# Kernel tuning notes

Measured on AMD Instinct MI355X. Metric: run time of the kernel, lower is better.

Reference implementation:

```python
import jax, jax.numpy as jnp
import numpy as np

N, E, B = 100000, 400000, 4096      # nodes, directed edges, graphs
P, d = 4, 49                        # phm_dim, per-component dim; D = P*d = 196
L = 3                               # message-passing layers
D1, D2 = 64, 32                     # downstream per-component dims (256/4, 128/4)


def setup_inputs():
    key = jax.random.key(0)
    ks = jax.random.split(key, 20)
    def nrm(k, shape, s=0.1):
        return jax.random.normal(k, shape, dtype=jnp.float32) * s
    return {
        "x": jax.random.randint(ks[0], (N, 9), 0, 119),
        "edge_index": jax.random.randint(ks[1], (2, E), 0, N),
        "edge_attr": jax.random.randint(ks[2], (E, 3), 0, 8),
        "batch": jnp.sort(jax.random.randint(ks[3], (N,), 0, B)),
        # encoders: summed categorical embeddings in hypercomplex form [*, P, d]
        "atom_emb": nrm(ks[4], (9, 119, P, d)),
        "bond_emb": nrm(ks[5], (L, 3, 8, P, d)),
        # per-layer PHM conv: contribution matrices A (phm rule) + component weights W
        "conv_A": nrm(ks[6], (L, P, P, P), 0.5),
        "conv_W": nrm(ks[7], (L, P, d, d)),
        "conv_b": jnp.zeros((L, P, d), jnp.float32),
        "mp_gamma": jnp.ones((L, P * d), jnp.float32),
        "mp_beta": jnp.zeros((L, P * d), jnp.float32),
        # soft-attention pooling: PHM linear + real transformer gate
        "pool_A": nrm(ks[8], (P, P, P), 0.5),
        "pool_W": nrm(ks[9], (P, d, d)),
        "pool_b": jnp.zeros((P, d), jnp.float32),
        "pool_rt_w": nrm(ks[10], (P,), 0.5),
        "pool_rt_b": jnp.zeros((d,), jnp.float32),
        # downstream PHM MLP 196 -> 256 -> 128 -> 4*1, then real trafo -> 1
        "dn_A": nrm(ks[11], (3, P, P, P), 0.5),
        "dn1_W": nrm(ks[12], (P, d, D1)),
        "dn1_b": jnp.zeros((P, D1), jnp.float32),
        "dn1_gamma": jnp.ones((P * D1,), jnp.float32),
        "dn1_beta": jnp.zeros((P * D1,), jnp.float32),
        "dn2_W": nrm(ks[13], (P, D1, D2)),
        "dn2_b": jnp.zeros((P, D2), jnp.float32),
        "dn2_gamma": jnp.ones((P * D2,), jnp.float32),
        "dn2_beta": jnp.zeros((P * D2,), jnp.float32),
        "dn3_W": nrm(ks[14], (P, D2, 1)),
        "dn3_b": jnp.zeros((P, 1), jnp.float32),
        "rt_w": nrm(ks[15], (P,), 0.5),
        "rt_b": jnp.zeros((1,), jnp.float32),
    }


def phm_linear(x, A, W, b):
    # PHM linear: y = x @ (sum_i kron(A_i, W_i)) + b, on [n, P, din] -> [n, P, dout]
    return jnp.einsum('nkp,ikj,ipq->njq', x, A, W) + b


def naive_bn(x, gamma, beta, eps=1e-5):
    # naive batch norm over the batch axis, per flattened hypercomplex feature
    n, p, dd = x.shape
    x2 = x.reshape(n, p * dd)
    mu = x2.mean(axis=0)
    var = x2.var(axis=0)
    x2 = (x2 - mu) * jax.lax.rsqrt(var + eps) * gamma + beta
    return x2.reshape(n, p, dd)


def reference(x, edge_index, edge_attr, batch, atom_emb, bond_emb,
              conv_A, conv_W, conv_b, mp_gamma, mp_beta,
              pool_A, pool_W, pool_b, pool_rt_w, pool_rt_b,
              dn_A, dn1_W, dn1_b, dn1_gamma, dn1_beta,
              dn2_W, dn2_b, dn2_gamma, dn2_beta, dn3_W, dn3_b, rt_w, rt_b):
    src, dst = edge_index[0], edge_index[1]
    # atom encoder: sum embeddings of 9 categorical features -> [N, P, d]
    h0 = atom_emb[jnp.arange(9), x].sum(axis=1)
    h = h0
    for l in range(L):  # small fixed layer count
        # bond encoder for this layer -> [E, P, d]
        e = bond_emb[l][jnp.arange(3), edge_attr].sum(axis=1)
        # message = x_j + e_ij (identity msg encoder); self-loop (zero edge feat) adds h
        m = h[src] + e
        agg = jax.ops.segment_sum(m, dst, num_segments=N) + h
        z = phm_linear(agg, conv_A[l], conv_W[l], conv_b[l])
        z = jax.nn.relu(naive_bn(z, mp_gamma[l], mp_beta[l]))
        h = z + h0  # skip-connect to first embedding (sc_type='first')
    # soft-attention pooling: real-valued sigmoid gate per node feature
    g = jax.nn.sigmoid(
        jnp.einsum('npk,p->nk', phm_linear(h, pool_A, pool_W, pool_b), pool_rt_w)
        + pool_rt_b)
    pooled = jax.ops.segment_sum(h * g[:, None, :], batch, num_segments=B)  # [B, P, d]
    # downstream PHM MLP with naive batch norm + relu
    z = jax.nn.relu(naive_bn(phm_linear(pooled, dn_A[0], dn1_W, dn1_b), dn1_gamma, dn1_beta))
    z = jax.nn.relu(naive_bn(phm_linear(z, dn_A[1], dn2_W, dn2_b), dn2_gamma, dn2_beta))
    o = phm_linear(z, dn_A[2], dn3_W, dn3_b)          # [B, P, 1]
    return jnp.einsum('npk,p->nk', o, rt_w) + rt_b    # [B, 1]
```

## Files before the change

### kernel.cpp

```cpp
#include <hip/hip_runtime.h>
#include <cstdint>
#include <cstddef>

#define N_NODES 100000
#define N_EDGES 400000
#define N_GRAPHS 4096
#define DF 196
#define DD 49
#define NPB 5
#define TST 200

typedef __bf16 bf16x8 __attribute__((ext_vector_type(8)));
typedef float f32x4 __attribute__((ext_vector_type(4)));

__device__ __forceinline__ unsigned short f2bf(float f) {
  unsigned int u = __float_as_uint(f);
  u = u + 0x7FFFu + ((u >> 16) & 1u);
  return (unsigned short)(u >> 16);
}
__device__ __forceinline__ float bf2f(unsigned short h) {
  return __uint_as_float(((unsigned int)h) << 16);
}

__global__ void convert_wfrag_kernel(const float* __restrict__ cA,
                                     const float* __restrict__ cW,
                                     unsigned short* __restrict__ wfrag) {
  int idx = blockIdx.x * blockDim.x + threadIdx.x;
  if (idx >= 3 * 100352) return;
  int l = idx / 100352;
  int r = idx - l * 100352;
  int ct = r / 7168; int r1 = r - ct * 7168;
  int ks = r1 / 1024; int r2 = r1 - ks * 1024;
  int h = r2 / 512;  int r3 = r2 - h * 512;
  int ln = r3 / 8;   int j = r3 - ln * 8;
  int col = ct * 16 + (ln & 15);
  int k = ks * 32 + (ln >> 4) * 8 + j;
  float v = 0.f;
  if (col < DF && k < DF) {
    int k4 = k / DD, p = k - (k / DD) * DD;
    int j4 = col / DD, q = col - (col / DD) * DD;
#pragma unroll
    for (int i = 0; i < 4; i++)
      v += cA[((l * 4 + i) * 4 + k4) * 4 + j4] * cW[((l * 4 + i) * DD + p) * DD + q];
  }
  unsigned short hi = f2bf(v);
  wfrag[idx] = (h == 0) ? hi : f2bf(v - bf2f(hi));
}

__global__ void build_gate_kernel(const float* __restrict__ pA, const float* __restrict__ pW,
                                  const float* __restrict__ pb, const float* __restrict__ rtw,
                                  const float* __restrict__ rtb,
                                  float* __restrict__ gateW, float* __restrict__ gbias) {
  int idx = blockIdx.x * blockDim.x + threadIdx.x;
  if (idx < DF * DD) {
    int r = idx / DD, q = idx - (idx / DD) * DD;
    int k = r / DD, p = r - (r / DD) * DD;
    float s = 0.f;
#pragma unroll
    for (int i = 0; i < 4; i++) {
      float aw = 0.f;
#pragma unroll
      for (int j = 0; j < 4; j++) aw += pA[(i * 4 + k) * 4 + j] * rtw[j];
      s += aw * pW[(i * DD + p) * DD + q];
    }
    gateW[idx] = s;
  } else if (idx < DF * DD + DD) {
    int q = idx - DF * DD;
    float s = rtb[q];
#pragma unroll
    for (int j = 0; j < 4; j++) s += rtw[j] * pb[j * DD + q];
    gbias[q] = s;
  }
}

__global__ void build_dn_kernel(const float* __restrict__ dnA,
                                const float* __restrict__ W1, const float* __restrict__ W2,
                                const float* __restrict__ W3,
                                float* __restrict__ M1, float* __restrict__ M2,
                                float* __restrict__ M3) {
  int idx = blockIdx.x * blockDim.x + threadIdx.x;
  const int n1 = DF * 256, n2 = 256 * 128, n3 = 128 * 4;
  if (idx < n1) {
    int r = idx >> 8, c = idx & 255;
    int k = r / DD, p = r - (r / DD) * DD;
    int j = c >> 6, Q = c & 63;
    float s = 0.f;
#pragma unroll
    for (int i = 0; i < 4; i++) s += dnA[i * 16 + k * 4 + j] * W1[(i * DD + p) * 64 + Q];
    M1[idx] = s;
  } else if (idx < n1 + n2) {
    int m = idx - n1;
    int r = m >> 7, c = m & 127;
    int k = r >> 6, p = r & 63, j = c >> 5, q = c & 31;
    float s = 0.f;
#pragma unroll
    for (int i = 0; i < 4; i++) s += dnA[64 + i * 16 + k * 4 + j] * W2[(i * 64 + p) * 32 + q];
    M2[m] = s;
  } else if (idx < n1 + n2 + n3) {
    int m = idx - n1 - n2;
    int r = m >> 2, j = m & 3;
    int k = r >> 5, p = r & 31;
    float s = 0.f;
#pragma unroll
    for (int i = 0; i < 4; i++) s += dnA[128 + i * 16 + k * 4 + j] * W3[i * 32 + p];
    M3[m] = s;
  }
}

__global__ void lut_kernel(const float* __restrict__ bond, float* __restrict__ lut) {
  int idx = blockIdx.x * blockDim.x + threadIdx.x;
  if (idx >= 3 * 512 * DF) return;
  int l = idx / (512 * DF);
  int r = idx - l * (512 * DF);
  int code = r / DF, c = r - (r / DF) * DF;
  int a0 = code & 7, a1 = (code >> 3) & 7, a2 = (code >> 6) & 7;
  lut[idx] = bond[((l * 3 + 0) * 8 + a0) * DF + c]
           + bond[((l * 3 + 1) * 8 + a1) * DF + c]
           + bond[((l * 3 + 2) * 8 + a2) * DF + c];
}

__global__ void hist_kernel(const int* __restrict__ dst, int* __restrict__ counts) {
  int e = blockIdx.x * blockDim.x + threadIdx.x;
  if (e < N_EDGES) atomicAdd(&counts[dst[e]], 1);
}

__global__ void scan_local_kernel(const int* __restrict__ counts, int* __restrict__ offs,
                                  int* __restrict__ bsum) {
  __shared__ int sm[256];
  int tid = threadIdx.x;
  int gid = blockIdx.x * 256 + tid;
  int v = (gid < N_NODES) ? counts[gid] : 0;
  sm[tid] = v;
  __syncthreads();
  for (int d = 1; d < 256; d <<= 1) {
    int add = (tid >= d) ? sm[tid - d] : 0;
    __syncthreads();
    sm[tid] += add;
    __syncthreads();
  }
  if (gid < N_NODES) offs[gid] = sm[tid] - v;
  if (tid == 255) bsum[blockIdx.x] = sm[255];
}

__global__ void scan_bsum_kernel(int* __restrict__ bsum, int* __restrict__ bpre, int nb) {
  __shared__ int sm[512];
  int tid = threadIdx.x;
  int v = (tid < nb) ? bsum[tid] : 0;
  sm[tid] = v;
  __syncthreads();
  for (int d = 1; d < 512; d <<= 1) {
    int add = (tid >= d) ? sm[tid - d] : 0;
    __syncthreads();
    sm[tid] += add;
    __syncthreads();
  }
  if (tid < nb) bpre[tid] = sm[tid] - v;
}

__global__ void add_off_kernel(int* __restrict__ offs, const int* __restrict__ bpre) {
  int gid = blockIdx.x * blockDim.x + threadIdx.x;
  if (gid < N_NODES) offs[gid] += bpre[gid >> 8];
  if (gid == 0) offs[N_NODES] = N_EDGES;
}

__global__ void scatter_kernel(const int* __restrict__ src, const int* __restrict__ dst,
                               const int* __restrict__ ea, int* __restrict__ counts,
                               const int* __restrict__ offs,
                               unsigned int* __restrict__ sorted) {
  int e = blockIdx.x * blockDim.x + threadIdx.x;
  if (e >= N_EDGES) return;
  int d = dst[e];
  int code = ea[e * 3 + 0] | (ea[e * 3 + 1] << 3) | (ea[e * 3 + 2] << 6);
  int pos = offs[d] + atomicSub(&counts[d], 1) - 1;
  sorted[pos] = (unsigned int)src[e] | ((unsigned int)code << 17);
}

__global__ void sortseg_kernel(const int* __restrict__ offs,
                               unsigned int* __restrict__ sorted) {
  int n = blockIdx.x * blockDim.x + threadIdx.x;
  if (n >= N_NODES) return;
  int s = offs[n], e = offs[n + 1];
  for (int i = s + 1; i < e; i++) {
    unsigned int v = sorted[i];
    int j = i - 1;
    while (j >= s && sorted[j] > v) { sorted[j + 1] = sorted[j]; j--; }
    sorted[j + 1] = v;
  }
}

__global__ void atom_enc_kernel(const int* __restrict__ x, const float* __restrict__ emb,
                                float* __restrict__ h0) {
  int idx = blockIdx.x * blockDim.x + threadIdx.x;
  if (idx >= N_NODES * DF) return;
  int n = idx / DF;
  int c = idx - n * DF;
  float s = 0.f;
#pragma unroll
  for (int f = 0; f < 9; f++) {
    int xi = x[n * 9 + f];
    s += emb[(f * 119 + xi) * DF + c];
  }
  h0[idx] = s;
}

__global__ __launch_bounds__(256)
void agg_kernel(const float* __restrict__ h, const int* __restrict__ offs,
                const unsigned int* __restrict__ sorted, const float* __restrict__ lut,
                unsigned short* __restrict__ tH, unsigned short* __restrict__ tL) {
  int t = threadIdx.x;
  int i = t / 49, q = t - i * 49;
  if (i >= NPB) return;
  int node = blockIdx.x * NPB + i;
  if (node >= N_NODES) return;
  const float4* h4 = (const float4*)h;
  const float4* l4 = (const float4*)lut;
  float4 acc = h4[(size_t)node * 49 + q];
  int s = offs[node], e = offs[node + 1];
  for (int k = s; k < e; k++) {
    unsigned int se = sorted[k];
    int srcn = se & 0x1FFFF;
    int code = se >> 17;
    float4 hv = h4[(size_t)srcn * 49 + q];
    float4 lv = l4[(size_t)code * 49 + q];
    acc.x += hv.x + lv.x;
    acc.y += hv.y + lv.y;
    acc.z += hv.z + lv.z;
    acc.w += hv.w + lv.w;
  }
  ushort4 hh, ll;
  hh.x = f2bf(acc.x); ll.x = f2bf(acc.x - bf2f(hh.x));
  hh.y = f2bf(acc.y); ll.y = f2bf(acc.y - bf2f(hh.y));
  hh.z = f2bf(acc.z); ll.z = f2bf(acc.z - bf2f(hh.z));
  hh.w = f2bf(acc.w); ll.w = f2bf(acc.w - bf2f(hh.w));
  size_t ob = (size_t)node * TST + q * 4;
  *(ushort4*)(tH + ob) = hh;
  *(ushort4*)(tL + ob) = ll;
  if (q == 48) {
    ushort4 z = make_ushort4(0, 0, 0, 0);
    *(ushort4*)(tH + (size_t)node * TST + 196) = z;
    *(ushort4*)(tL + (size_t)node * TST + 196) = z;
  }
}

__global__ __launch_bounds__(256, 2)
void conv_mfma_kernel(unsigned short* __restrict__ tH,
                      unsigned short* __restrict__ tL,
                      const unsigned short* __restrict__ wfrag,
                      const float* __restrict__ bias,
                      float* __restrict__ stats) {
  __shared__ __align__(16) unsigned short smW[28672];
  const int t = threadIdx.x;
  const int lane = t & 63;
  const int w = t >> 6;
  const int li = lane & 15;
  const int rg = lane >> 4;
  const int rowbase = blockIdx.x * 128 + w * 32;

  f32x4 acc[2][14];
#pragma unroll
  for (int rt = 0; rt < 2; rt++)
#pragma unroll
    for (int ct = 0; ct < 14; ct++) acc[rt][ct] = (f32x4){0.f, 0.f, 0.f, 0.f};

  uint4 aH0[2], aL0[2], aH1[2], aL1[2];

#define LOADA(ks, aH, aL)                                                      \
  {                                                                            \
    _Pragma("unroll") for (int rt = 0; rt < 2; rt++) {                         \
      size_t o = (size_t)(rowbase + rt * 16 + li) * TST + (ks) * 32 + rg * 8;  \
      aH[rt] = *(const uint4*)(tH + o);                                        \
      aL[rt] = *(const uint4*)(tL + o);                                        \
    }                                                                          \
  }

#define COMPUTE(ksl, aH, aL)                                                   \
  {                                                                            \
    _Pragma("unroll") for (int ct = 0; ct < 14; ct++) {                        \
      bf16x8 bh = *(const bf16x8*)(smW + (((ct * 2 + (ksl)) * 2 + 0) * 512 + lane * 8)); \
      bf16x8 bl = *(const bf16x8*)(smW + (((ct * 2 + (ksl)) * 2 + 1) * 512 + lane * 8)); \
      _Pragma("unroll") for (int rt = 0; rt < 2; rt++) {                       \
        bf16x8 ah = *(const bf16x8*)&aH[rt];                                   \
        bf16x8 al = *(const bf16x8*)&aL[rt];                                   \
        acc[rt][ct] = __builtin_amdgcn_mfma_f32_16x16x32_bf16(ah, bh, acc[rt][ct], 0, 0, 0); \
        acc[rt][ct] = __builtin_amdgcn_mfma_f32_16x16x32_bf16(al, bh, acc[rt][ct], 0, 0, 0); \
        acc[rt][ct] = __builtin_amdgcn_mfma_f32_16x16x32_bf16(ah, bl, acc[rt][ct], 0, 0, 0); \
      }                                                                        \
    }                                                                          \
  }

#define STAGE_PAIR(p)                                                          \
  {                                                                            \
    _Pragma("unroll") for (int f0 = 0; f0 < 14; f0++) {                        \
      int f = f0 * 256 + t;                                                    \
      int ln = f & 63, g = f >> 6;                                             \
      int hh = g & 1, g2 = g >> 1;                                             \
      int ksl = g2 & 1, ct = g2 >> 1;                                          \
      *(uint4*)(smW + (((ct * 2 + ksl) * 2 + hh) * 512 + ln * 8)) =            \
          *(const uint4*)(wfrag + (((size_t)(ct * 7 + 2 * (p) + ksl) * 2 + hh) * 512 + ln * 8)); \
    }                                                                          \
  }

  LOADA(0, aH0, aL0);
  STAGE_PAIR(0);
  __syncthreads();
  LOADA(1, aH1, aL1);
  COMPUTE(0, aH0, aL0);
  LOADA(2, aH0, aL0);
  COMPUTE(1, aH1, aL1);
  __syncthreads();
  STAGE_PAIR(1);
  __syncthreads();
  LOADA(3, aH1, aL1);
  COMPUTE(0, aH0, aL0);
  LOADA(4, aH0, aL0);
  COMPUTE(1, aH1, aL1);
  __syncthreads();
  STAGE_PAIR(2);
  __syncthreads();
  LOADA(5, aH1, aL1);
  COMPUTE(0, aH0, aL0);
  LOADA(6, aH0, aL0);
  COMPUTE(1, aH1, aL1);
  __syncthreads();
  {
#pragma unroll
    for (int f0 = 0; f0 < 7; f0++) {
      int f = f0 * 256 + t;
      int ln = f & 63, g = f >> 6;
      int hh = g & 1, ct = g >> 1;
      *(uint4*)(smW + (((ct * 2) * 2 + hh) * 512 + ln * 8)) =
          *(const uint4*)(wfrag + (((size_t)(ct * 7 + 6) * 2 + hh) * 512 + ln * 8));
    }
  }
  __syncthreads();
  COMPUTE(0, aH0, aL0);
  __syncthreads();

  float* redS = (float*)smW;
  float* redQ = redS + 4 * 224;
#pragma unroll
  for (int ct = 0; ct < 14; ct++) {
    int c = ct * 16 + li;
    float bv = (c < DF) ? bias[c] : 0.f;
    float part = 0.f, psq = 0.f;
#pragma unroll
    for (int rt = 0; rt < 2; rt++) {
#pragma unroll
      for (int r = 0; r < 4; r++) {
        int gr = rowbase + rt * 16 + rg * 4 + r;
        float y = acc[rt][ct][r] + bv;
        if (gr < N_NODES && c < DF) {
          part += y; psq += y * y;
          unsigned short hi = f2bf(y);
          unsigned short lo = f2bf(y - bf2f(hi));
          size_t ob = (size_t)gr * TST + c;
          tH[ob] = hi;
          tL[ob] = lo;
        }
      }
    }
    part += __shfl_xor(part, 16, 64); part += __shfl_xor(part, 32, 64);
    psq  += __shfl_xor(psq , 16, 64); psq  += __shfl_xor(psq , 32, 64);
    if (rg == 0) { redS[w * 224 + c] = part; redQ[w * 224 + c] = psq; }
  }
  __syncthreads();
  if (t < DF) {
    float s1 = redS[t] + redS[224 + t] + redS[448 + t] + redS[672 + t];
    float s2 = redQ[t] + redQ[224 + t] + redQ[448 + t] + redQ[672 + t];
    atomicAdd(&stats[t], s1);
    atomicAdd(&stats[DF + t], s2);
  }
#undef LOADA
#undef COMPUTE
#undef STAGE_PAIR
}

__global__ void bn_relu_split_kernel(const unsigned short* __restrict__ tH,
                                     const unsigned short* __restrict__ tL,
                                     const float* __restrict__ stats,
                                     const float* __restrict__ gamma,
                                     const float* __restrict__ beta,
                                     const float* __restrict__ h0,
                                     float* __restrict__ h) {
  int idx = blockIdx.x * blockDim.x + threadIdx.x;
  if (idx >= N_NODES * DD) return;
  int n = idx / DD, q = idx - (idx / DD) * DD;
  size_t ib = (size_t)n * TST + q * 4;
  ushort4 hv = *(const ushort4*)(tH + ib);
  ushort4 lv = *(const ushort4*)(tL + ib);
  size_t fb = (size_t)n * DF + q * 4;
  float4 sk = *(const float4*)(h0 + fb);
  int c = q * 4;
  const float invN = 1.f / N_NODES;
  float4 o;
  {
    float z = bf2f(hv.x) + bf2f(lv.x);
    float mu = stats[c + 0] * invN;
    float var = stats[DF + c + 0] * invN - mu * mu;
    o.x = fmaxf((z - mu) * rsqrtf(var + 1e-5f) * gamma[c + 0] + beta[c + 0], 0.f) + sk.x;
  }
  {
    float z = bf2f(hv.y) + bf2f(lv.y);
    float mu = stats[c + 1] * invN;
    float var = stats[DF + c + 1] * invN - mu * mu;
    o.y = fmaxf((z - mu) * rsqrtf(var + 1e-5f) * gamma[c + 1] + beta[c + 1], 0.f) + sk.y;
  }
  {
    float z = bf2f(hv.z) + bf2f(lv.z);
    float mu = stats[c + 2] * invN;
    float var = stats[DF + c + 2] * invN - mu * mu;
    o.z = fmaxf((z - mu) * rsqrtf(var + 1e-5f) * gamma[c + 2] + beta[c + 2], 0.f) + sk.z;
  }
  {
    float z = bf2f(hv.w) + bf2f(lv.w);
    float mu = stats[c + 3] * invN;
    float var = stats[DF + c + 3] * invN - mu * mu;
    o.w = fmaxf((z - mu) * rsqrtf(var + 1e-5f) * gamma[c + 3] + beta[c + 3], 0.f) + sk.w;
  }
  *(float4*)(h + fb) = o;
}

template<int S, int MODE>
__launch_bounds__(256)
__global__ void gemm_kernel(const float* X, const float* __restrict__ W,
                            const float* __restrict__ bias, float* Y,
                            float* __restrict__ stats, int Nrows, int K, int NC) {
  constexpr int WN = S * 64;
  __shared__ __align__(16) float At[32][64];
  __shared__ __align__(16) float Wl[32][WN];
  const int t = threadIdx.x;
  const int tx = t & 15;
  const int ty = t >> 4;
  const int r0 = blockIdx.x * 64;

  float acc[S][4][4];
#pragma unroll
  for (int s = 0; s < S; s++)
#pragma unroll
    for (int i = 0; i < 4; i++)
#pragma unroll
      for (int j = 0; j < 4; j++) acc[s][i][j] = 0.f;

  const int lr = t >> 2;
  const int kb = (t & 3) * 8;
  constexpr int TPR = S * 16;
  const int cw = (t % TPR) * 4;
  const int kr = t / TPR;
  constexpr int RPP = 256 / TPR;
  constexpr int PASSES = 32 / RPP;

  for (int k0 = 0; k0 < K; k0 += 32) {
    {
      const int gr = r0 + lr;
      const float* xp = X + (size_t)gr * K + k0 + kb;
      if (gr < Nrows && (k0 + kb + 7) < K) {
        float4 v0 = *(const float4*)(xp);
        float4 v1 = *(const float4*)(xp + 4);
        At[kb + 0][lr] = v0.x; At[kb + 1][lr] = v0.y;
        At[kb + 2][lr] = v0.z; At[kb + 3][lr] = v0.w;
        At[kb + 4][lr] = v1.x; At[kb + 5][lr] = v1.y;
        At[kb + 6][lr] = v1.z; At[kb + 7][lr] = v1.w;
      } else {
#pragma unroll
        for (int i = 0; i < 8; i++) {
          int kk = kb + i;
          float v = 0.f;
          if (gr < Nrows && (k0 + kk) < K) v = xp[i];
          At[kk][lr] = v;
        }
      }
    }
#pragma unroll
    for (int ps = 0; ps < PASSES; ps++) {
      int kk = kr + ps * RPP;
      int gk = k0 + kk;
      if (gk < K && (cw + 3) < NC && ((NC & 3) == 0)) {
        float4 v = *(const float4*)(W + (size_t)gk * NC + cw);
        Wl[kk][cw + 0] = v.x; Wl[kk][cw + 1] = v.y;
        Wl[kk][cw + 2] = v.z; Wl[kk][cw + 3] = v.w;
      } else {
#pragma unroll
        for (int j = 0; j < 4; j++) {
          int c = cw + j;
          float v = 0.f;
          if (gk < K && c < NC) v = W[(size_t)gk * NC + c];
          Wl[kk][c] = v;
        }
      }
    }
    __syncthreads();
#pragma unroll 4
    for (int kk = 0; kk < 32; kk++) {
      float4 a = *(const float4*)&At[kk][ty * 4];
      float av[4] = {a.x, a.y, a.z, a.w};
#pragma unroll
      for (int s = 0; s < S; s++) {
        float4 w = *(const float4*)&Wl[kk][s * 64 + tx * 4];
        float wv[4] = {w.x, w.y, w.z, w.w};
#pragma unroll
        for (int i = 0; i < 4; i++)
#pragma unroll
          for (int j = 0; j < 4; j++)
            acc[s][i][j] = fmaf(av[i], wv[j], acc[s][i][j]);
      }
    }
    __syncthreads();
  }

#pragma unroll
  for (int s = 0; s < S; s++)
#pragma unroll
    for (int j = 0; j < 4; j++) {
      int c = s * 64 + tx * 4 + j;
      float bv = (c < NC) ? bias[c] : 0.f;
#pragma unroll
      for (int i = 0; i < 4; i++) {
        float y = acc[s][i][j] + bv;
        if (MODE == 1) y = 1.f / (1.f + __expf(-y));
        acc[s][i][j] = y;
      }
    }
#pragma unroll
  for (int i = 0; i < 4; i++) {
    int gr = r0 + ty * 4 + i;
    if (gr < Nrows) {
#pragma unroll
      for (int s = 0; s < S; s++)
#pragma unroll
        for (int j = 0; j < 4; j++) {
          int c = s * 64 + tx * 4 + j;
          if (c < NC) Y[(size_t)gr * NC + c] = acc[s][i][j];
        }
    }
  }
  if (MODE == 0) {
    float* red = &Wl[0][0];
    __syncthreads();
#pragma unroll
    for (int s = 0; s < S; s++)
#pragma unroll
      for (int j = 0; j < 4; j++) {
        float p = 0.f;
#pragma unroll
        for (int i = 0; i < 4; i++)
          if ((r0 + ty * 4 + i) < Nrows) p += acc[s][i][j];
        red[ty * WN + s * 64 + tx * 4 + j] = p;
      }
    __syncthreads();
    if (t < WN) {
      float tot = 0.f;
#pragma unroll
      for (int yy = 0; yy < 16; yy++) tot += red[yy * WN + t];
      if (t < NC) atomicAdd(&stats[t], tot);
    }
    __syncthreads();
#pragma unroll
    for (int s = 0; s < S; s++)
#pragma unroll
      for (int j = 0; j < 4; j++) {
        float p = 0.f;
#pragma unroll
        for (int i = 0; i < 4; i++)
          if ((r0 + ty * 4 + i) < Nrows) p += acc[s][i][j] * acc[s][i][j];
        red[ty * WN + s * 64 + tx * 4 + j] = p;
      }
    __syncthreads();
    if (t < WN) {
      float tot = 0.f;
#pragma unroll
      for (int yy = 0; yy < 16; yy++) tot += red[yy * WN + t];
      if (t < NC) atomicAdd(&stats[NC + t], tot);
    }
  }
}

__global__ void bn_relu_kernel(const float* __restrict__ z, const float* __restrict__ stats,
                               const float* __restrict__ gamma, const float* __restrict__ beta,
                               float* __restrict__ out,
                               int total, int NC, float invN) {
  int idx = blockIdx.x * blockDim.x + threadIdx.x;
  if (idx >= total) return;
  int c = idx % NC;
  float mu = stats[c] * invN;
  float var = stats[NC + c] * invN - mu * mu;
  float v = (z[idx] - mu) * rsqrtf(var + 1e-5f) * gamma[c] + beta[c];
  out[idx] = fmaxf(v, 0.f);
}

__device__ __forceinline__ int lower_bound_dev(const int* a, int n, int v) {
  int lo = 0, hi = n;
  while (lo < hi) { int mid = (lo + hi) >> 1; if (a[mid] < v) lo = mid + 1; else hi = mid; }
  return lo;
}

__global__ void pool_kernel(const float* __restrict__ h, const float* __restrict__ g,
                            const int* __restrict__ batch, float* __restrict__ pooled) {
  int b = blockIdx.x;
  __shared__ int bounds[2];
  if (threadIdx.x == 0) {
    bounds[0] = lower_bound_dev(batch, N_NODES, b);
    bounds[1] = lower_bound_dev(batch, N_NODES, b + 1);
  }
  __syncthreads();
  int c = threadIdx.x;
  if (c >= DF) return;
  int s = bounds[0], e = bounds[1];
  int q = c % DD;
  float acc = 0.f;
  for (int n = s; n < e; n++)
    acc = fmaf(h[(size_t)n * DF + c], g[(size_t)n * DD + q], acc);
  pooled[(size_t)b * DF + c] = acc;
}

__global__ void final_kernel(const float* __restrict__ z2, const float* __restrict__ M3,
                             const float* __restrict__ b3, const float* __restrict__ rtw,
                             const float* __restrict__ rtb, float* __restrict__ out) {
  __shared__ float sM[128 * 4];
  __shared__ float srw[4];
  __shared__ float srb;
  int t = threadIdx.x;
  for (int i = t; i < 512; i += 256) sM[i] = M3[i];
  if (t < 4) srw[t] = rtw[t];
  if (t == 4) srb = rtb[0];
  __syncthreads();
  int b = blockIdx.x * blockDim.x + t;
  if (b >= N_GRAPHS) return;
  float o0 = b3[0], o1 = b3[1], o2 = b3[2], o3 = b3[3];
  const float* zp = z2 + (size_t)b * 128;
  for (int p = 0; p < 128; p++) {
    float v = zp[p];
    o0 = fmaf(v, sM[p * 4 + 0], o0);
    o1 = fmaf(v, sM[p * 4 + 1], o1);
    o2 = fmaf(v, sM[p * 4 + 2], o2);
    o3 = fmaf(v, sM[p * 4 + 3], o3);
  }
  out[b] = srb + o0 * srw[0] + o1 * srw[1] + o2 * srw[2] + o3 * srw[3];
}

extern "C" void kernel_launch(void* const* d_in, const int* in_sizes, int n_in,
                              void* d_out, int out_size, void* d_ws, size_t ws_size,
                              hipStream_t stream) {
  (void)in_sizes; (void)n_in; (void)out_size; (void)ws_size;
  const int* x          = (const int*)d_in[0];
  const int* edge_index = (const int*)d_in[1];
  const int* edge_attr  = (const int*)d_in[2];
  const int* batch      = (const int*)d_in[3];
  const float* atom_emb = (const float*)d_in[4];
  const float* bond_emb = (const float*)d_in[5];
  const float* conv_A   = (const float*)d_in[6];
  const float* conv_W   = (const float*)d_in[7];
  const float* conv_b   = (const float*)d_in[8];
  const float* mp_gamma = (const float*)d_in[9];
  const float* mp_beta  = (const float*)d_in[10];
  const float* pool_A   = (const float*)d_in[11];
  const float* pool_W   = (const float*)d_in[12];
  const float* pool_b   = (const float*)d_in[13];
  const float* pool_rt_w = (const float*)d_in[14];
  const float* pool_rt_b = (const float*)d_in[15];
  const float* dn_A     = (const float*)d_in[16];
  const float* dn1_W    = (const float*)d_in[17];
  const float* dn1_b    = (const float*)d_in[18];
  const float* dn1_gamma = (const float*)d_in[19];
  const float* dn1_beta = (const float*)d_in[20];
  const float* dn2_W    = (const float*)d_in[21];
  const float* dn2_b    = (const float*)d_in[22];
  const float* dn2_gamma = (const float*)d_in[23];
  const float* dn2_beta = (const float*)d_in[24];
  const float* dn3_W    = (const float*)d_in[25];
  const float* dn3_b    = (const float*)d_in[26];
  const float* rt_w     = (const float*)d_in[27];
  const float* rt_b     = (const float*)d_in[28];
  float* out = (float*)d_out;

  char* ws = (char*)d_ws;
  size_t off = 0;
  auto alloc = [&](size_t bytes) -> char* {
    char* p = ws + off;
    off = (off + bytes + 255) & ~(size_t)255;
    return p;
  };
  const size_t HBYTES = (size_t)N_NODES * DF * sizeof(float);
  float* h0 = (float*)alloc(HBYTES);
  float* h  = (float*)alloc(HBYTES);
  unsigned short* tH = (unsigned short*)alloc((size_t)N_NODES * TST * 2 + 4096);
  unsigned short* tL = (unsigned short*)alloc((size_t)N_NODES * TST * 2 + 4096);
  float* g      = (float*)tH;
  float* pooled = (float*)((char*)tH + (((size_t)N_NODES * DD * 4 + 255) & ~(size_t)255));
  float* z1     = (float*)((char*)pooled + (((size_t)N_GRAPHS * DF * 4 + 255) & ~(size_t)255));
  float* z2     = (float*)((char*)z1 + (((size_t)N_GRAPHS * 256 * 4 + 255) & ~(size_t)255));
  unsigned short* wfrag = (unsigned short*)alloc((size_t)3 * 100352 * 2);
  float* gateW  = (float*)alloc(DF * DD * 4);
  float* gbias  = (float*)alloc(64 * 4);
  float* M1     = (float*)alloc(DF * 256 * 4);
  float* M2     = (float*)alloc(256 * 128 * 4);
  float* M3     = (float*)alloc(128 * 4 * 4);
  float* stats  = (float*)alloc(2048 * 4);
  int*  counts  = (int*)alloc(N_NODES * 4);
  int*  offs    = (int*)alloc((N_NODES + 1) * 4);
  unsigned int* sorted = (unsigned int*)alloc((size_t)N_EDGES * 4);
  float* lut    = (float*)alloc((size_t)3 * 512 * DF * 4);
  int*  bsum    = (int*)alloc(512 * 4);
  int*  bpre    = (int*)alloc(512 * 4);

  const int* src = edge_index;
  const int* dst = edge_index + N_EDGES;
  const int NB = (N_NODES + 255) / 256;

  hipMemsetAsync(stats, 0, 2048 * 4, stream);
  hipMemsetAsync(counts, 0, N_NODES * 4, stream);

  convert_wfrag_kernel<<<(3 * 100352 + 255) / 256, 256, 0, stream>>>(conv_A, conv_W, wfrag);
  build_gate_kernel<<<(DF * DD + DD + 255) / 256, 256, 0, stream>>>(
      pool_A, pool_W, pool_b, pool_rt_w, pool_rt_b, gateW, gbias);
  build_dn_kernel<<<(DF * 256 + 256 * 128 + 128 * 4 + 255) / 256, 256, 0, stream>>>(
      dn_A, dn1_W, dn2_W, dn3_W, M1, M2, M3);
  lut_kernel<<<(3 * 512 * DF + 255) / 256, 256, 0, stream>>>(bond_emb, lut);

  hist_kernel<<<(N_EDGES + 255) / 256, 256, 0, stream>>>(dst, counts);
  scan_local_kernel<<<NB, 256, 0, stream>>>(counts, offs, bsum);
  scan_bsum_kernel<<<1, 512, 0, stream>>>(bsum, bpre, NB);
  add_off_kernel<<<NB, 256, 0, stream>>>(offs, bpre);
  scatter_kernel<<<(N_EDGES + 255) / 256, 256, 0, stream>>>(
      src, dst, edge_attr, counts, offs, sorted);
  sortseg_kernel<<<NB, 256, 0, stream>>>(offs, sorted);

  atom_enc_kernel<<<(N_NODES * DF + 255) / 256, 256, 0, stream>>>(x, atom_emb, h0);

  const int NCONV = (N_NODES + 127) / 128;
  for (int l = 0; l < 3; l++) {
    const float* hl = (l == 0) ? h0 : h;
    agg_kernel<<<(N_NODES + NPB - 1) / NPB, 256, 0, stream>>>(
        hl, offs, sorted, lut + (size_t)l * 512 * DF, tH, tL);
    float* st = stats + l * 392;
    conv_mfma_kernel<<<NCONV, 256, 0, stream>>>(
        tH, tL, wfrag + (size_t)l * 100352, conv_b + (size_t)l * DF, st);
    bn_relu_split_kernel<<<(N_NODES * DD + 255) / 256, 256, 0, stream>>>(
        tH, tL, st, mp_gamma + l * DF, mp_beta + l * DF, h0, h);
  }

  gemm_kernel<1, 1><<<(N_NODES + 63) / 64, 256, 0, stream>>>(
      h, gateW, gbias, g, nullptr, N_NODES, DF, DD);
  pool_kernel<<<N_GRAPHS, 256, 0, stream>>>(h, g, batch, pooled);

  gemm_kernel<4, 0><<<(N_GRAPHS + 63) / 64, 256, 0, stream>>>(
      pooled, M1, dn1_b, z1, stats + 1176, N_GRAPHS, DF, 256);
  bn_relu_kernel<<<(N_GRAPHS * 256 + 255) / 256, 256, 0, stream>>>(
      z1, stats + 1176, dn1_gamma, dn1_beta, z1, N_GRAPHS * 256, 256, 1.f / N_GRAPHS);
  gemm_kernel<2, 0><<<(N_GRAPHS + 63) / 64, 256, 0, stream>>>(
      z1, M2, dn2_b, z2, stats + 1688, N_GRAPHS, 256, 128);
  bn_relu_kernel<<<(N_GRAPHS * 128 + 255) / 256, 256, 0, stream>>>(
      z2, stats + 1688, dn2_gamma, dn2_beta, z2, N_GRAPHS * 128, 128, 1.f / N_GRAPHS);
  final_kernel<<<(N_GRAPHS + 255) / 256, 256, 0, stream>>>(z2, M3, dn3_b, rt_w, rt_b, out);
}
```

Baseline: 930.4 us.

## Deepen A-operand prefetch and stage GEMM epilogue through LDS for coalesced stores

The PHM GEMM kernel now prefetches four K-slices of the A operand up front instead of two, so more global loads are in flight before the first MFMA. The epilogue no longer writes scattered 2-byte hi/lo values straight to global memory. Each half of the tile is first written into shared memory, then copied out as coalesced 16-byte row stores, with pad columns zeroed. This adds register pressure and extra LDS round trips and barriers in exchange for wide global stores.

```diff
diff --git a/kernel.cpp b/kernel.cpp
--- a/kernel.cpp
+++ b/kernel.cpp
@@ -262,7 +262,7 @@
 #pragma unroll
     for (int ct = 0; ct < 14; ct++) acc[rt][ct] = (f32x4){0.f, 0.f, 0.f, 0.f};
 
-  uint4 aH0[2], aL0[2], aH1[2], aL1[2];
+  uint4 h0b[2], l0b[2], h1b[2], l1b[2], h2b[2], l2b[2], h3b[2], l3b[2];
 
 #define LOADA(ks, aH, aL)                                                      \
   {                                                                            \
@@ -300,27 +300,27 @@
     }                                                                          \
   }
 
-  LOADA(0, aH0, aL0);
+  LOADA(0, h0b, l0b);
+  LOADA(1, h1b, l1b);
+  LOADA(2, h2b, l2b);
+  LOADA(3, h3b, l3b);
   STAGE_PAIR(0);
   __syncthreads();
-  LOADA(1, aH1, aL1);
-  COMPUTE(0, aH0, aL0);
-  LOADA(2, aH0, aL0);
-  COMPUTE(1, aH1, aL1);
+  COMPUTE(0, h0b, l0b);
+  LOADA(4, h0b, l0b);
+  COMPUTE(1, h1b, l1b);
   __syncthreads();
   STAGE_PAIR(1);
   __syncthreads();
-  LOADA(3, aH1, aL1);
-  COMPUTE(0, aH0, aL0);
-  LOADA(4, aH0, aL0);
-  COMPUTE(1, aH1, aL1);
+  COMPUTE(0, h2b, l2b);
+  LOADA(5, h1b, l1b);
+  COMPUTE(1, h3b, l3b);
   __syncthreads();
   STAGE_PAIR(2);
   __syncthreads();
-  LOADA(5, aH1, aL1);
-  COMPUTE(0, aH0, aL0);
-  LOADA(6, aH0, aL0);
-  COMPUTE(1, aH1, aL1);
+  COMPUTE(0, h0b, l0b);
+  LOADA(6, h2b, l2b);
+  COMPUTE(1, h1b, l1b);
   __syncthreads();
   {
 #pragma unroll
@@ -333,35 +333,62 @@
     }
   }
   __syncthreads();
-  COMPUTE(0, aH0, aL0);
-  __syncthreads();
-
+  COMPUTE(0, h2b, l2b);
+
+  float part[14], psq[14];
+#pragma unroll
+  for (int ct = 0; ct < 14; ct++) { part[ct] = 0.f; psq[ct] = 0.f; }
+
+  unsigned short* lhi = smW;
+  unsigned short* llo = smW + 64 * 224;
+
+#pragma unroll
+  for (int half = 0; half < 2; half++) {
+    __syncthreads();
+    if ((w >> 1) == half) {
+      int rl0 = (w & 1) * 32;
+#pragma unroll
+      for (int ct = 0; ct < 14; ct++) {
+        int c = ct * 16 + li;
+        float bv = (c < DF) ? bias[c] : 0.f;
+#pragma unroll
+        for (int rt = 0; rt < 2; rt++) {
+#pragma unroll
+          for (int r = 0; r < 4; r++) {
+            int row = rl0 + rt * 16 + rg * 4 + r;
+            int gr = rowbase + rt * 16 + rg * 4 + r;
+            float y = acc[rt][ct][r] + bv;
+            if (gr < N_NODES && c < DF) { part[ct] += y; psq[ct] += y * y; }
+            unsigned short hi = f2bf(y);
+            lhi[row * 224 + c] = hi;
+            llo[row * 224 + c] = f2bf(y - bf2f(hi));
+          }
+        }
+      }
+    }
+    __syncthreads();
+    for (int idx = t; idx < 1600; idx += 256) {
+      int row = idx / 25, u = idx - (idx / 25) * 25;
+      int gr = blockIdx.x * 128 + half * 64 + row;
+      if (gr < N_NODES) {
+        uint4 vh = *(const uint4*)(lhi + row * 224 + u * 8);
+        uint4 vl = *(const uint4*)(llo + row * 224 + u * 8);
+        if (u == 24) { vh.z = 0u; vh.w = 0u; vl.z = 0u; vl.w = 0u; }
+        *(uint4*)(tH + (size_t)gr * TST + u * 8) = vh;
+        *(uint4*)(tL + (size_t)gr * TST + u * 8) = vl;
+      }
+    }
+  }
+
+  __syncthreads();
   float* redS = (float*)smW;
   float* redQ = redS + 4 * 224;
 #pragma unroll
   for (int ct = 0; ct < 14; ct++) {
-    int c = ct * 16 + li;
-    float bv = (c < DF) ? bias[c] : 0.f;
-    float part = 0.f, psq = 0.f;
-#pragma unroll
-    for (int rt = 0; rt < 2; rt++) {
-#pragma unroll
-      for (int r = 0; r < 4; r++) {
-        int gr = rowbase + rt * 16 + rg * 4 + r;
-        float y = acc[rt][ct][r] + bv;
-        if (gr < N_NODES && c < DF) {
-          part += y; psq += y * y;
-          unsigned short hi = f2bf(y);
-          unsigned short lo = f2bf(y - bf2f(hi));
-          size_t ob = (size_t)gr * TST + c;
-          tH[ob] = hi;
-          tL[ob] = lo;
-        }
-      }
-    }
-    part += __shfl_xor(part, 16, 64); part += __shfl_xor(part, 32, 64);
-    psq  += __shfl_xor(psq , 16, 64); psq  += __shfl_xor(psq , 32, 64);
-    if (rg == 0) { redS[w * 224 + c] = part; redQ[w * 224 + c] = psq; }
+    float p = part[ct], q = psq[ct];
+    p += __shfl_xor(p, 16, 64); p += __shfl_xor(p, 32, 64);
+    q += __shfl_xor(q, 16, 64); q += __shfl_xor(q, 32, 64);
+    if (rg == 0) { redS[w * 224 + ct * 16 + li] = p; redQ[w * 224 + ct * 16 + li] = q; }
   }
   __syncthreads();
   if (t < DF) {
```

Measured after the change: 892.5 us. 1.04x faster.
